# Optimization experiments

Hardware: AMD Instinct MI355X
Metric: run time of the kernel (lower is better)

The kernel has to match this reference:

```python
import jax, jax.numpy as jnp
import numpy as np

B, N, NAB, NF, NG = 2, 512, 128, 128, 32
CUTOFF = 5.0


def ssp(x):
    # shifted softplus: ln(1+e^x) - ln 2
    return jax.nn.softplus(x) - jnp.log(2.0).astype(x.dtype)


def setup_inputs() -> dict:
    key = jax.random.key(0)
    ks = jax.random.split(key, 10)
    offsets = jnp.linspace(0.0, CUTOFF, NG)
    widths = jnp.full((NG,), offsets[1] - offsets[0])
    s = 0.05
    return {
        "r": jax.random.normal(ks[0], (B, N, NAB), jnp.float32),
        "e": jax.random.uniform(ks[1], (B, N, N), jnp.float32),
        "A": jax.random.uniform(ks[2], (B, N, N), jnp.float32),
        "offsets": offsets,
        "widths": widths,
        "W_df1": jax.random.normal(ks[3], (NG, NG), jnp.float32) * s,
        "b_df1": jnp.zeros((NG,), jnp.float32),
        "W_df2": jax.random.normal(ks[4], (NG, NF), jnp.float32) * s,
        "b_df2": jnp.zeros((NF,), jnp.float32),
        "W_af": jax.random.normal(ks[5], (NAB, NF), jnp.float32) * s,
        "W_d1": jax.random.normal(ks[6], (NF, NAB), jnp.float32) * s,
        "b_d1": jnp.zeros((NAB,), jnp.float32),
        "W_d2": jax.random.normal(ks[7], (NAB, NAB), jnp.float32) * s,
        "b_d2": jnp.zeros((NAB,), jnp.float32),
    }


def reference(r, e, A, offsets, widths, W_df1, b_df1, W_df2, b_df2,
              W_af, W_d1, b_d1, W_d2, b_d2):
    # Gaussian smearing (trainable offsets/widths, non-centered)
    coeff = -0.5 / (widths ** 2)                       # [G]
    diff = e[:, :, :, None] - offsets[None, None, None, :]  # [B,N,N,G]
    es = jnp.exp(coeff * diff ** 2)                    # [B,N,N,G]
    # DistanceFilter1 output is computed then discarded (faithful to source)
    _ = ssp(es @ W_df1 + b_df1)
    W = es @ W_df2 + b_df2                             # [B,N,N,F]
    rf = r @ W_af                                      # [B,N,F]
    # cfconv: broadcast-multiply-reduce over neighbor axis j
    y = jnp.einsum("bjf,bij,bijf->bif", rf, A, W)      # [B,N,F]
    y = ssp(y @ W_d1 + b_d1)                           # [B,N,NAB]
    y = y @ W_d2 + b_d2                                # [B,N,NAB]
    return y
```

## Files before the change

### kernel.cpp

```cpp
#include <hip/hip_runtime.h>
#include <math.h>

#define BB 2
#define NN 512
#define NAB 128
#define NF 128
#define NG 32

typedef _Float16 f16;
typedef f16 f16x8 __attribute__((ext_vector_type(8)));
typedef f16 f16x4 __attribute__((ext_vector_type(4)));
typedef float f32x4 __attribute__((ext_vector_type(4)));

#define TS 520
#define SS 132

__global__ __launch_bounds__(256) void prep_rf(const float* __restrict__ r,
                                               const float* __restrict__ W_af,
                                               f16* __restrict__ rfT) {
    const int tid = threadIdx.x;
    const int r0  = blockIdx.x * 4;
    const int b   = r0 >> 9;
    const int j0  = r0 & 511;

    __shared__ float sr[4][128];
    __shared__ f16   st[128][8];

    for (int t = tid; t < 512; t += 256)
        sr[t >> 7][t & 127] = r[(r0 + (t >> 7)) * NAB + (t & 127)];
    __syncthreads();

    const int f  = tid & 127;
    const int rh = tid >> 7;
    float a0 = 0.f, a1 = 0.f;
    #pragma unroll 8
    for (int k = 0; k < NAB; ++k) {
        const float wv = W_af[k * NF + f];
        a0 += sr[2 * rh + 0][k] * wv;
        a1 += sr[2 * rh + 1][k] * wv;
    }
    st[f][2 * rh + 0] = (f16)a0;
    st[f][2 * rh + 1] = (f16)a1;
    __syncthreads();

    if (tid < 128) {
        f16x4 v;
        v[0] = st[tid][0]; v[1] = st[tid][1]; v[2] = st[tid][2]; v[3] = st[tid][3];
        *(f16x4*)(rfT + b * (NF * NN) + tid * NN + j0) = v;
    }
}

__global__ __launch_bounds__(256, 4) void fused_kernel(
    const float* __restrict__ e, const float* __restrict__ A,
    const f16*  __restrict__ rfT,
    const float* __restrict__ offsets, const float* __restrict__ widths,
    const float* __restrict__ W_df2, const float* __restrict__ b_df2,
    const float* __restrict__ W_d1,  const float* __restrict__ b_d1,
    const float* __restrict__ W_d2,  const float* __restrict__ b_d2,
    float* __restrict__ out) {

    const int bi  = blockIdx.x;
    const int b   = bi >> 9;
    const int tid = threadIdx.x;
    const int w    = tid >> 6;
    const int lane = tid & 63;
    const int q    = lane >> 4;
    const int n    = lane & 15;

    __shared__ __align__(16) float smem[2 * 33 * SS];
    __shared__ float sconst[64];
    __shared__ float sy[128];
    __shared__ float spart[2][128];

    f16* Tsh = (f16*)smem;

    if (tid < NG) {
        sconst[tid] = offsets[tid];
        const float wd = widths[tid];
        sconst[32 + tid] = -0.5f / (wd * wd);
    }

    const int j0 = (tid & 127) * 4;
    const float4 ev = *(const float4*)(e + bi * NN + j0);
    const float4 av = *(const float4*)(A + bi * NN + j0);
    __syncthreads();

    #pragma unroll
    for (int i = 0; i < 16; ++i) {
        const int g = (tid >> 7) + 2 * i;
        const float off = sconst[g];
        const float cf  = sconst[32 + g];
        const float d0 = ev.x - off, d1 = ev.y - off;
        const float d2 = ev.z - off, d3 = ev.w - off;
        f16x4 v;
        v[0] = (f16)(av.x * __expf(cf * d0 * d0));
        v[1] = (f16)(av.y * __expf(cf * d1 * d1));
        v[2] = (f16)(av.z * __expf(cf * d2 * d2));
        v[3] = (f16)(av.w * __expf(cf * d3 * d3));
        *(f16x4*)(Tsh + g * TS + j0) = v;
    }
    if (tid < 128) {
        f16x4 v;
        v[0] = (f16)av.x; v[1] = (f16)av.y; v[2] = (f16)av.z; v[3] = (f16)av.w;
        *(f16x4*)(Tsh + 32 * TS + j0) = v;
    }
    __syncthreads();

    const int kh = w >> 1;
    const int nh = w & 1;

    f32x4 acc[3][4];
    #pragma unroll
    for (int mt = 0; mt < 3; ++mt)
        #pragma unroll
        for (int nt = 0; nt < 4; ++nt)
            acc[mt][nt] = (f32x4){0.f, 0.f, 0.f, 0.f};

    const f16* Abase = Tsh + n * TS + kh * 256 + q * 8;
    const f16* A2base = Tsh + 32 * TS + kh * 256 + q * 8;
    const f16* Bbase = rfT + (size_t)b * (NF * NN) + (nh * 64 + n) * NN + kh * 256 + q * 8;

    #pragma unroll
    for (int kk = 0; kk < 8; ++kk) {
        f16x8 bcur[4];
        #pragma unroll
        for (int nt = 0; nt < 4; ++nt)
            bcur[nt] = *(const f16x8*)(Bbase + kk * 32 + nt * 16 * NN);
        const f16x8 a0 = *(const f16x8*)(Abase + kk * 32);
        const f16x8 a1 = *(const f16x8*)(Abase + 16 * TS + kk * 32);
        const f16x8 a2 = *(const f16x8*)(A2base + kk * 32);
        #pragma unroll
        for (int nt = 0; nt < 4; ++nt) {
            acc[0][nt] = __builtin_amdgcn_mfma_f32_16x16x32_f16(a0, bcur[nt], acc[0][nt], 0, 0, 0);
            acc[1][nt] = __builtin_amdgcn_mfma_f32_16x16x32_f16(a1, bcur[nt], acc[1][nt], 0, 0, 0);
            acc[2][nt] = __builtin_amdgcn_mfma_f32_16x16x32_f16(a2, bcur[nt], acc[2][nt], 0, 0, 0);
        }
    }

    __syncthreads();
    float* Sp = smem + kh * (33 * SS);
    #pragma unroll
    for (int mt = 0; mt < 2; ++mt)
        #pragma unroll
        for (int nt = 0; nt < 4; ++nt)
            #pragma unroll
            for (int rr = 0; rr < 4; ++rr)
                Sp[(mt * 16 + q * 4 + rr) * SS + nh * 64 + nt * 16 + n] = acc[mt][nt][rr];
    if (q == 0) {
        #pragma unroll
        for (int nt = 0; nt < 4; ++nt)
            Sp[32 * SS + nh * 64 + nt * 16 + n] = acc[2][nt][0];
    }
    __syncthreads();

    {
        const float* S0 = smem;
        const float* S1 = smem + 33 * SS;
        const int f = tid & 127;
        float a;
        if (tid < 128) {
            a = b_df2[f] * (S0[32 * SS + f] + S1[32 * SS + f]);
            #pragma unroll
            for (int g = 0; g < 16; ++g)
                a += W_df2[g * NF + f] * (S0[g * SS + f] + S1[g * SS + f]);
        } else {
            a = 0.f;
            #pragma unroll
            for (int g = 16; g < 32; ++g)
                a += W_df2[g * NF + f] * (S0[g * SS + f] + S1[g * SS + f]);
        }
        spart[tid >> 7][f] = a;
    }
    __syncthreads();
    if (tid < 128) sy[tid] = spart[0][tid] + spart[1][tid];
    __syncthreads();

    {
        const int f = tid & 127, hh = tid >> 7;
        float a = 0.f;
        #pragma unroll 8
        for (int k = hh * 64; k < hh * 64 + 64; ++k)
            a += sy[k] * W_d1[k * NAB + f];
        spart[hh][f] = a;
    }
    __syncthreads();
    float hreg = 0.f;
    if (tid < NAB) {
        const float x = spart[0][tid] + spart[1][tid] + b_d1[tid];
        const float sp = (x > 0.f) ? (x + log1pf(__expf(-x))) : log1pf(__expf(x));
        hreg = sp - 0.69314718055994530942f;
    }
    __syncthreads();
    if (tid < NAB) sy[tid] = hreg;
    __syncthreads();

    {
        const int f = tid & 127, hh = tid >> 7;
        float a = 0.f;
        #pragma unroll 8
        for (int k = hh * 64; k < hh * 64 + 64; ++k)
            a += sy[k] * W_d2[k * NAB + f];
        spart[hh][f] = a;
    }
    __syncthreads();
    if (tid < NAB)
        out[bi * NAB + tid] = spart[0][tid] + spart[1][tid] + b_d2[tid];
}

extern "C" void kernel_launch(void* const* d_in, const int* in_sizes, int n_in,
                              void* d_out, int out_size, void* d_ws, size_t ws_size,
                              hipStream_t stream) {
    const float* r       = (const float*)d_in[0];
    const float* e       = (const float*)d_in[1];
    const float* A       = (const float*)d_in[2];
    const float* offsets = (const float*)d_in[3];
    const float* widths  = (const float*)d_in[4];
    const float* W_df2   = (const float*)d_in[7];
    const float* b_df2   = (const float*)d_in[8];
    const float* W_af    = (const float*)d_in[9];
    const float* W_d1    = (const float*)d_in[10];
    const float* b_d1    = (const float*)d_in[11];
    const float* W_d2    = (const float*)d_in[12];
    const float* b_d2    = (const float*)d_in[13];
    float* out = (float*)d_out;

    f16* rfT = (f16*)d_ws;

    prep_rf<<<BB * NN / 4, 256, 0, stream>>>(r, W_af, rfT);
    fused_kernel<<<BB * NN, 256, 0, stream>>>(e, A, rfT, offsets, widths,
                                              W_df2, b_df2, W_d1, b_d1,
                                              W_d2, b_d2, out);
}
```

Baseline: 110.5 us.

## Use MFMA for dense epilogue layers and fdot2 for A-row sum

The two 128x128 dense layers in the per-row epilogue now run as fp16 MFMA matrix-vector products against transposed fp16 weights, which prep_rf produces. This replaces scalar fp32 loops that each needed an extra partial-sum reduction and barrier. The third MFMA tile, which only carried the A-weighted row sum, is replaced by packed fdot2 accumulation plus a cross-lane shuffle reduction, and the shared-memory footprint shrinks. The main loop unroll drops to 2 to ease register pressure. The trade-off is fp16 rounding of intermediate activations and weights, plus broadcast-row MFMAs that waste most of each output tile.

New measurement: 114.9 us. 4.0% more time.

```diff
diff --git a/kernel.cpp b/kernel.cpp
--- a/kernel.cpp
+++ b/kernel.cpp
@@ -10,18 +10,37 @@
 typedef _Float16 f16;
 typedef f16 f16x8 __attribute__((ext_vector_type(8)));
 typedef f16 f16x4 __attribute__((ext_vector_type(4)));
+typedef f16 f16x2 __attribute__((ext_vector_type(2)));
 typedef float f32x4 __attribute__((ext_vector_type(4)));
 
 #define TS 520
 #define SS 132
 
+union F8 { f16x8 v; f16x2 h[4]; };
+
 __global__ __launch_bounds__(256) void prep_rf(const float* __restrict__ r,
                                                const float* __restrict__ W_af,
-                                               f16* __restrict__ rfT) {
+                                               const float* __restrict__ W_d1,
+                                               const float* __restrict__ W_d2,
+                                               f16* __restrict__ rfT,
+                                               f16* __restrict__ W1T,
+                                               f16* __restrict__ W2T) {
     const int tid = threadIdx.x;
     const int r0  = blockIdx.x * 4;
     const int b   = r0 >> 9;
     const int j0  = r0 & 511;
+
+    if (blockIdx.x < 32) {
+        const int m  = blockIdx.x >> 4;
+        const float* Wsrc = m ? W_d2 : W_d1;
+        f16* Wdst = m ? W2T : W1T;
+        const int k0 = (blockIdx.x & 15) * 8 + (tid >> 7) * 4;
+        const int f  = tid & 127;
+        f16x4 v;
+        #pragma unroll
+        for (int t = 0; t < 4; ++t) v[t] = (f16)Wsrc[(k0 + t) * NAB + f];
+        *(f16x4*)(Wdst + f * NAB + k0) = v;
+    }
 
     __shared__ float sr[4][128];
     __shared__ f16   st[128][8];
@@ -53,10 +72,10 @@
 __global__ __launch_bounds__(256, 4) void fused_kernel(
     const float* __restrict__ e, const float* __restrict__ A,
     const f16*  __restrict__ rfT,
+    const f16*  __restrict__ W1T, const f16* __restrict__ W2T,
     const float* __restrict__ offsets, const float* __restrict__ widths,
     const float* __restrict__ W_df2, const float* __restrict__ b_df2,
-    const float* __restrict__ W_d1,  const float* __restrict__ b_d1,
-    const float* __restrict__ W_d2,  const float* __restrict__ b_d2,
+    const float* __restrict__ b_d1,  const float* __restrict__ b_d2,
     float* __restrict__ out) {
 
     const int bi  = blockIdx.x;
@@ -67,10 +86,12 @@
     const int q    = lane >> 4;
     const int n    = lane & 15;
 
-    __shared__ __align__(16) float smem[2 * 33 * SS];
+    __shared__ __align__(16) float smem[33 * TS / 2];
+    __shared__ float s32p[256];
     __shared__ float sconst[64];
-    __shared__ float sy[128];
-    __shared__ float spart[2][128];
+    __shared__ float sh1[128];
+    __shared__ __align__(16) f16 yh16[128];
+    __shared__ __align__(16) f16 hh16[128];
 
     f16* Tsh = (f16*)smem;
 
@@ -109,36 +130,39 @@
     const int kh = w >> 1;
     const int nh = w & 1;
 
-    f32x4 acc[3][4];
-    #pragma unroll
-    for (int mt = 0; mt < 3; ++mt)
+    f32x4 acc[2][4];
+    float s32a[4] = {0.f, 0.f, 0.f, 0.f};
+    #pragma unroll
+    for (int mt = 0; mt < 2; ++mt)
         #pragma unroll
         for (int nt = 0; nt < 4; ++nt)
             acc[mt][nt] = (f32x4){0.f, 0.f, 0.f, 0.f};
 
     const f16* Abase = Tsh + n * TS + kh * 256 + q * 8;
-    const f16* A2base = Tsh + 32 * TS + kh * 256 + q * 8;
+    const f16* Rbase = Tsh + 32 * TS + kh * 256 + q * 8;
     const f16* Bbase = rfT + (size_t)b * (NF * NN) + (nh * 64 + n) * NN + kh * 256 + q * 8;
 
-    #pragma unroll
+    #pragma unroll 2
     for (int kk = 0; kk < 8; ++kk) {
-        f16x8 bcur[4];
-        #pragma unroll
-        for (int nt = 0; nt < 4; ++nt)
-            bcur[nt] = *(const f16x8*)(Bbase + kk * 32 + nt * 16 * NN);
+        F8 bc[4];
+        #pragma unroll
+        for (int nt = 0; nt < 4; ++nt)
+            bc[nt].v = *(const f16x8*)(Bbase + kk * 32 + nt * 16 * NN);
         const f16x8 a0 = *(const f16x8*)(Abase + kk * 32);
         const f16x8 a1 = *(const f16x8*)(Abase + 16 * TS + kk * 32);
-        const f16x8 a2 = *(const f16x8*)(A2base + kk * 32);
+        F8 avv; avv.v = *(const f16x8*)(Rbase + kk * 32);
         #pragma unroll
         for (int nt = 0; nt < 4; ++nt) {
-            acc[0][nt] = __builtin_amdgcn_mfma_f32_16x16x32_f16(a0, bcur[nt], acc[0][nt], 0, 0, 0);
-            acc[1][nt] = __builtin_amdgcn_mfma_f32_16x16x32_f16(a1, bcur[nt], acc[1][nt], 0, 0, 0);
-            acc[2][nt] = __builtin_amdgcn_mfma_f32_16x16x32_f16(a2, bcur[nt], acc[2][nt], 0, 0, 0);
+            acc[0][nt] = __builtin_amdgcn_mfma_f32_16x16x32_f16(a0, bc[nt].v, acc[0][nt], 0, 0, 0);
+            acc[1][nt] = __builtin_amdgcn_mfma_f32_16x16x32_f16(a1, bc[nt].v, acc[1][nt], 0, 0, 0);
+            #pragma unroll
+            for (int t = 0; t < 4; ++t)
+                s32a[nt] = __builtin_amdgcn_fdot2(avv.h[t], bc[nt].h[t], s32a[nt], false);
         }
     }
 
     __syncthreads();
-    float* Sp = smem + kh * (33 * SS);
+    float* Sp = smem + kh * (32 * SS);
     #pragma unroll
     for (int mt = 0; mt < 2; ++mt)
         #pragma unroll
@@ -146,65 +170,71 @@
             #pragma unroll
             for (int rr = 0; rr < 4; ++rr)
                 Sp[(mt * 16 + q * 4 + rr) * SS + nh * 64 + nt * 16 + n] = acc[mt][nt][rr];
-    if (q == 0) {
-        #pragma unroll
-        for (int nt = 0; nt < 4; ++nt)
-            Sp[32 * SS + nh * 64 + nt * 16 + n] = acc[2][nt][0];
-    }
-    __syncthreads();
-
-    {
+    #pragma unroll
+    for (int nt = 0; nt < 4; ++nt) {
+        s32a[nt] += __shfl_xor(s32a[nt], 16);
+        s32a[nt] += __shfl_xor(s32a[nt], 32);
+    }
+    if (lane < 16) {
+        #pragma unroll
+        for (int nt = 0; nt < 4; ++nt)
+            s32p[kh * 128 + nh * 64 + nt * 16 + lane] = s32a[nt];
+    }
+    __syncthreads();
+
+    if (tid < 128) {
         const float* S0 = smem;
-        const float* S1 = smem + 33 * SS;
-        const int f = tid & 127;
-        float a;
-        if (tid < 128) {
-            a = b_df2[f] * (S0[32 * SS + f] + S1[32 * SS + f]);
-            #pragma unroll
-            for (int g = 0; g < 16; ++g)
-                a += W_df2[g * NF + f] * (S0[g * SS + f] + S1[g * SS + f]);
-        } else {
-            a = 0.f;
-            #pragma unroll
-            for (int g = 16; g < 32; ++g)
-                a += W_df2[g * NF + f] * (S0[g * SS + f] + S1[g * SS + f]);
+        const float* S1 = smem + 32 * SS;
+        float a = b_df2[tid] * (s32p[tid] + s32p[128 + tid]);
+        #pragma unroll 8
+        for (int g = 0; g < NG; ++g)
+            a += W_df2[g * NF + tid] * (S0[g * SS + tid] + S1[g * SS + tid]);
+        yh16[tid] = (f16)a;
+    }
+    __syncthreads();
+
+    f32x4 m1[2];
+    m1[0] = (f32x4){0.f, 0.f, 0.f, 0.f};
+    m1[1] = (f32x4){0.f, 0.f, 0.f, 0.f};
+    #pragma unroll
+    for (int kk = 0; kk < 4; ++kk) {
+        const f16x8 af = *(const f16x8*)(yh16 + kk * 32 + q * 8);
+        #pragma unroll
+        for (int nt = 0; nt < 2; ++nt) {
+            const f16x8 bf = *(const f16x8*)(W1T + (w * 32 + nt * 16 + n) * NAB + kk * 32 + q * 8);
+            m1[nt] = __builtin_amdgcn_mfma_f32_16x16x32_f16(af, bf, m1[nt], 0, 0, 0);
         }
-        spart[tid >> 7][f] = a;
-    }
-    __syncthreads();
-    if (tid < 128) sy[tid] = spart[0][tid] + spart[1][tid];
-    __syncthreads();
-
-    {
-        const int f = tid & 127, hh = tid >> 7;
-        float a = 0.f;
-        #pragma unroll 8
-        for (int k = hh * 64; k < hh * 64 + 64; ++k)
-            a += sy[k] * W_d1[k * NAB + f];
-        spart[hh][f] = a;
-    }
-    __syncthreads();
-    float hreg = 0.f;
-    if (tid < NAB) {
-        const float x = spart[0][tid] + spart[1][tid] + b_d1[tid];
+    }
+    if (lane < 16) {
+        sh1[w * 32 + 0  + lane] = m1[0][0];
+        sh1[w * 32 + 16 + lane] = m1[1][0];
+    }
+    __syncthreads();
+
+    if (tid < 128) {
+        const float x = sh1[tid] + b_d1[tid];
         const float sp = (x > 0.f) ? (x + log1pf(__expf(-x))) : log1pf(__expf(x));
-        hreg = sp - 0.69314718055994530942f;
-    }
-    __syncthreads();
-    if (tid < NAB) sy[tid] = hreg;
-    __syncthreads();
-
-    {
-        const int f = tid & 127, hh = tid >> 7;
-        float a = 0.f;
-        #pragma unroll 8
-        for (int k = hh * 64; k < hh * 64 + 64; ++k)
-            a += sy[k] * W_d2[k * NAB + f];
-        spart[hh][f] = a;
-    }
-    __syncthreads();
-    if (tid < NAB)
-        out[bi * NAB + tid] = spart[0][tid] + spart[1][tid] + b_d2[tid];
+        hh16[tid] = (f16)(sp - 0.69314718055994530942f);
+    }
+    __syncthreads();
+
+    f32x4 m2[2];
+    m2[0] = (f32x4){0.f, 0.f, 0.f, 0.f};
+    m2[1] = (f32x4){0.f, 0.f, 0.f, 0.f};
+    #pragma unroll
+    for (int kk = 0; kk < 4; ++kk) {
+        const f16x8 af = *(const f16x8*)(hh16 + kk * 32 + q * 8);
+        #pragma unroll
+        for (int nt = 0; nt < 2; ++nt) {
+            const f16x8 bf = *(const f16x8*)(W2T + (w * 32 + nt * 16 + n) * NAB + kk * 32 + q * 8);
+            m2[nt] = __builtin_amdgcn_mfma_f32_16x16x32_f16(af, bf, m2[nt], 0, 0, 0);
+        }
+    }
+    if (lane < 16) {
+        const int f0 = w * 32 + lane;
+        out[bi * NAB + f0]      = m2[0][0] + b_d2[f0];
+        out[bi * NAB + f0 + 16] = m2[1][0] + b_d2[f0 + 16];
+    }
 }
 
 extern "C" void kernel_launch(void* const* d_in, const int* in_sizes, int n_in,
@@ -225,9 +255,11 @@
     float* out = (float*)d_out;
 
     f16* rfT = (f16*)d_ws;
-
-    prep_rf<<<BB * NN / 4, 256, 0, stream>>>(r, W_af, rfT);
-    fused_kernel<<<BB * NN, 256, 0, stream>>>(e, A, rfT, offsets, widths,
-                                              W_df2, b_df2, W_d1, b_d1,
-                                              W_d2, b_d2, out);
+    f16* W1T = rfT + BB * NF * NN;
+    f16* W2T = W1T + NAB * NAB;
+
+    prep_rf<<<BB * NN / 4, 256, 0, stream>>>(r, W_af, W_d1, W_d2, rfT, W1T, W2T);
+    fused_kernel<<<BB * NN, 256, 0, stream>>>(e, A, rfT, W1T, W2T,
+                                              offsets, widths, W_df2, b_df2,
+                                              b_d1, b_d2, out);
 }
```
